# Performance work log

Hardware: AMD Instinct MI355X
Metric: run time of the kernel (lower is better)

Reference implementation:

```python
import jax, jax.numpy as jnp
import numpy as np
import math

H, W = 512, 1024
PS = 2
H_p, W_p = H // PS, W // PS
N = 9
C_IN, C_OUT = 128, 64
GROUPS = 32
B = 2
EPS_GN = 1e-5


def _make_grid():
    # Replicates LatDeform2xDown buffers: centers + sec(lat)-scaled 3x3 offsets.
    pr = np.arange(H_p, dtype=np.float32) * PS + (PS - 1) / 2
    pc = np.arange(W_p, dtype=np.float32) * PS + (PS - 1) / 2
    cy = pr / (H - 1) * 2 - 1
    cx = pc / (W - 1) * 2 - 1
    centers = np.stack([np.broadcast_to(cx[None, :], (H_p, W_p)),
                        np.broadcast_to(cy[:, None], (H_p, W_p))], axis=-1)  # (H_p,W_p,2)
    delta = math.pi / (H - 1)  # drop_south_pole = False
    lat = math.pi / 2 - pr * delta
    sec_max = W / 4.0
    sec = np.clip(1.0 / np.cos(lat), -sec_max, sec_max).astype(np.float32)
    ky, kx = np.meshgrid(np.array([-1.0, 0.0, 1.0], np.float32),
                         np.array([-1.0, 0.0, 1.0], np.float32), indexing='ij')
    kxf, kyf = kx.flatten(), ky.flatten()
    dx = (kxf[None, :] * sec[:, None]) / (W - 1) * 2          # (H_p, 9)
    dy = np.broadcast_to(kyf[None, :], (H_p, N)) / (H - 1) * 2  # (H_p, 9)
    offsets = np.stack([dx, dy], axis=-1)                      # (H_p, 9, 2)
    locs = centers[:, :, None, :] + offsets[:, None, :, :]     # (H_p, W_p, 9, 2)
    return jnp.asarray(locs.reshape(-1, 2).astype(np.float32))


def group_norm(x, gamma, beta, groups, eps=EPS_GN):
    b, c, h, w = x.shape
    xg = x.reshape(b, groups, c // groups, h, w)
    mu = xg.mean(axis=(2, 3, 4), keepdims=True)
    var = ((xg - mu) ** 2).mean(axis=(2, 3, 4), keepdims=True)
    xn = ((xg - mu) * jax.lax.rsqrt(var + eps)).reshape(b, c, h, w)
    return xn * gamma[None, :, None, None] + beta[None, :, None, None]


def setup_inputs() -> dict:
    key = jax.random.key(0)
    ks = jax.random.split(key, 3)
    x = jax.random.normal(ks[0], (B, C_IN, H_p, W_p), dtype=jnp.float32)
    w_conv = jax.random.normal(ks[1], (N * C_OUT, C_IN), dtype=jnp.float32) * 0.02
    w_post = jax.random.normal(ks[2], (C_OUT, C_OUT), dtype=jnp.float32) * 0.05
    return {
        'x': x,
        'grid': _make_grid(),
        'gamma1': jnp.ones((C_IN,), jnp.float32),
        'beta1': jnp.zeros((C_IN,), jnp.float32),
        'w_conv': w_conv,
        'splat_bias': jnp.zeros((C_OUT,), jnp.float32),
        'w_post': w_post,
        'b_post': jnp.zeros((C_OUT,), jnp.float32),
        'gamma2': jnp.ones((C_OUT,), jnp.float32),
        'beta2': jnp.zeros((C_OUT,), jnp.float32),
    }


def reference(x, grid, gamma1, beta1, w_conv, splat_bias, w_post, b_post, gamma2, beta2):
    b = x.shape[0]
    # norm + 1x1 conv (no bias): Wx part of the Wx+b split
    h = group_norm(x, gamma1, beta1, GROUPS)
    vals = jnp.einsum('oc,bchw->bohw', w_conv, h)                 # (B, 9*C, H_p, W_p)
    vals = vals.reshape(b, C_OUT, N, H_p, W_p).transpose(0, 1, 3, 4, 2)
    vals = vals.reshape(b, C_OUT, H_p * W_p * N)                  # (B, C, M)

    # bilinear splat coordinates
    px = (grid[:, 0] + 1.0) * 0.5 * (W - 1)                       # (M,)
    py = (grid[:, 1] + 1.0) * 0.5 * (H - 1)
    x0 = jnp.floor(px).astype(jnp.int32)
    y0 = jnp.floor(py).astype(jnp.int32)
    x1, y1 = x0 + 1, y0 + 1
    fx = px - x0.astype(px.dtype)
    fy = py - y0.astype(py.dtype)
    w00 = (1 - fx) * (1 - fy)
    w01 = (1 - fx) * fy
    w10 = fx * (1 - fy)
    w11 = fx * fy
    x0w = x0 % W
    x1w = x1 % W
    half_W = W // 2

    def polar_wrap(yi, xi):
        past_n = yi < 0
        past_s = yi >= H
        yi = jnp.where(past_n, -yi, yi)
        yi = jnp.where(past_s, 2 * H - yi, yi)
        xi = jnp.where(past_n | past_s, (xi + half_W) % W, xi)
        return jnp.clip(yi, 0, H - 1), xi

    num = jnp.zeros((b, C_OUT, H * W), x.dtype)
    den = jnp.zeros((H * W,), x.dtype)  # identical across batch in the original
    for wt, yi, xi in ((w00, y0, x0w), (w01, y1, x0w), (w10, y0, x1w), (w11, y1, x1w)):
        yi, xi = polar_wrap(yi, xi)
        idx = yi * W + xi                                          # (M,)
        num = num.at[:, :, idx].add(vals * wt[None, None, :])
        den = den.at[idx].add(wt)

    out = num / jnp.clip(den, 1e-8)[None, None, :]
    out = out.reshape(b, C_OUT, H, W) + splat_bias[None, :, None, None]
    # post: 1x1 conv + GroupNorm + exact GELU
    out = jnp.einsum('oc,bchw->bohw', w_post, out) + b_post[None, :, None, None]
    out = group_norm(out, gamma2, beta2, GROUPS)
    return jax.nn.gelu(out, approximate=False)
```

## Files before the change

### kernel.cpp

```cpp
#include <hip/hip_runtime.h>
#include <cstdint>
#include <cstddef>

#define H_   512
#define W_   1024
#define HP_  256
#define WP_  512
#define NTAP 9
#define CIN  128
#define COUT 64
#define HWP  (HP_*WP_)
#define MIDX (HWP*NTAP)
#define HW_  (H_*W_)

typedef __attribute__((ext_vector_type(8))) short bhalf8_t;
typedef __attribute__((ext_vector_type(4))) float floatx4_t;

__device__ __forceinline__ unsigned short f2bf(float f) {
    unsigned u = __float_as_uint(f);
    u += 0x7fffu + ((u >> 16) & 1u);
    return (unsigned short)(u >> 16);
}
__device__ __forceinline__ unsigned cvt_pk_bf16(float lo, float hi) {
    unsigned r;
    asm("v_cvt_pk_bf16_f32 %0, %1, %2" : "=v"(r) : "v"(lo), "v"(hi));
    return r;
}

__global__ __launch_bounds__(256) void k0_prep(
    const float* __restrict__ w_conv, const float* __restrict__ w_post,
    const float* __restrict__ sbias,  const float* __restrict__ b_post,
    float* __restrict__ wfold, float* __restrict__ sb2,
    float* __restrict__ gnzero ) {
    int idx = blockIdx.x * 256 + threadIdx.x;
    if (idx < 73728) {
        int r = idx >> 7, ci = idx & 127;
        int n = r >> 6, o = r & 63;
        float acc = 0.f;
        #pragma unroll 8
        for (int op = 0; op < 64; ++op)
            acc = fmaf(w_post[o*64 + op], w_conv[(op*9 + n)*128 + ci], acc);
        wfold[idx] = acc;
    } else if (idx < 73728 + 64) {
        int o = idx - 73728;
        float acc = b_post[o];
        for (int op = 0; op < 64; ++op)
            acc = fmaf(w_post[o*64 + op], sbias[op], acc);
        sb2[o] = acc;
    } else if (idx < 73728 + 64 + 256) {
        gnzero[idx - (73728 + 64)] = 0.f;
    }
}

__global__ __launch_bounds__(256) void k1_stats(const float* __restrict__ x,
                                                float* __restrict__ gnsum1) {
    __shared__ float red[512];
    int bid = blockIdx.x;
    int b = bid >> 8, rem = bid & 255;
    int g = rem >> 3, slice = rem & 7;
    const float4* xp = (const float4*)x + (size_t)(b*CIN + g*4) * (HWP/4) + (size_t)slice*16384;
    float s = 0.f, s2 = 0.f;
    for (int i = threadIdx.x; i < 16384; i += 256) {
        float4 v = xp[i];
        s  += v.x + v.y + v.z + v.w;
        s2 += v.x*v.x + v.y*v.y + v.z*v.z + v.w*v.w;
    }
    red[threadIdx.x] = s; red[256 + threadIdx.x] = s2;
    __syncthreads();
    for (int off = 128; off > 0; off >>= 1) {
        if (threadIdx.x < off) {
            red[threadIdx.x] += red[threadIdx.x + off];
            red[256 + threadIdx.x] += red[256 + threadIdx.x + off];
        }
        __syncthreads();
    }
    if (threadIdx.x == 0) {
        atomicAdd(&gnsum1[(b*32 + g)*2],     red[0]);
        atomicAdd(&gnsum1[(b*32 + g)*2 + 1], red[256]);
    }
}

__global__ void k1b_coef(const float* __restrict__ gnsum1,
                         const float* __restrict__ gamma1, const float* __restrict__ beta1,
                         float* __restrict__ acoef, float* __restrict__ bcoef) {
    int t = threadIdx.x;
    int b = t >> 7, c = t & 127, g = c >> 2;
    float s1 = gnsum1[(b*32+g)*2], s2 = gnsum1[(b*32+g)*2+1];
    const float inv = 1.f / 524288.f;
    float mean = s1 * inv;
    float var  = s2 * inv - mean*mean;
    float rstd = rsqrtf(var + 1e-5f);
    float a = gamma1[c] * rstd;
    acoef[t] = a;
    bcoef[t] = beta1[c] - mean * a;
}

__global__ __launch_bounds__(256) void k1c_scale(
    const float* __restrict__ wfold, const float* __restrict__ acoef,
    const float* __restrict__ bcoef,
    unsigned short* __restrict__ w2b, float* __restrict__ vb) {
    int b = blockIdx.y;
    int idx = blockIdx.x * 256 + threadIdx.x;
    if (idx < 73728) {
        int c = idx & 127;
        w2b[b*73728 + idx] = f2bf(wfold[idx] * acoef[b*128 + c]);
    } else if (idx < 73728 + 576) {
        int r = idx - 73728;
        float acc = 0.f;
        #pragma unroll 8
        for (int c = 0; c < 128; ++c)
            acc = fmaf(wfold[r*128 + c], bcoef[b*128 + c], acc);
        vb[b*576 + r] = acc;
    }
}

__global__ __launch_bounds__(256) void k2_conv(
    const float* __restrict__ x, const unsigned short* __restrict__ w2b,
    const float* __restrict__ vb,
    unsigned short* __restrict__ vals) {
    __shared__ unsigned short Bs[128*136];
    __shared__ unsigned short Cs[128*72];
    int b   = blockIdx.y;
    int tile = blockIdx.x;
    int pr  = tile >> 2, pcb = (tile & 3) << 7;
    int tid = threadIdx.x;

    for (int task = tid; task < 2048; task += 256) {
        int p = task & 127, c0 = (task >> 7) << 3;
        const float* xp = &x[(size_t)(b*CIN + c0)*HWP + (size_t)pr*WP_ + pcb + p];
        float v0 = xp[0];
        float v1 = xp[HWP];
        float v2 = xp[2*HWP];
        float v3 = xp[3*HWP];
        float v4 = xp[4*HWP];
        float v5 = xp[5*HWP];
        float v6 = xp[6*HWP];
        float v7 = xp[7*HWP];
        uint4 t;
        t.x = cvt_pk_bf16(v0, v1);
        t.y = cvt_pk_bf16(v2, v3);
        t.z = cvt_pk_bf16(v4, v5);
        t.w = cvt_pk_bf16(v6, v7);
        *(uint4*)&Bs[p*136 + c0] = t;
    }
    __syncthreads();

    int wave = tid >> 6, lane = tid & 63;
    int l15 = lane & 15, lq = lane >> 4;

    bhalf8_t bfr[2][4];
    #pragma unroll
    for (int ptl = 0; ptl < 2; ++ptl) {
        int p = (wave*2 + ptl)*16 + l15;
        #pragma unroll
        for (int ks = 0; ks < 4; ++ks)
            bfr[ptl][ks] = *(const bhalf8_t*)&Bs[p*136 + ks*32 + lq*8];
    }

    const unsigned short* wb = w2b + (size_t)b*73728;
    const float* vbb = vb + b*576;

    for (int n = 0; n < 9; ++n) {
        floatx4_t acc[2][4];
        #pragma unroll
        for (int rt = 0; rt < 4; ++rt) {
            float4 vbv = *(const float4*)&vbb[n*64 + rt*16 + lq*4];
            floatx4_t a0; a0[0] = vbv.x; a0[1] = vbv.y; a0[2] = vbv.z; a0[3] = vbv.w;
            acc[0][rt] = a0; acc[1][rt] = a0;
        }
        #pragma unroll
        for (int ks = 0; ks < 4; ++ks) {
            bhalf8_t af[4];
            #pragma unroll
            for (int rt = 0; rt < 4; ++rt)
                af[rt] = *(const bhalf8_t*)&wb[(n*64 + rt*16 + l15)*128 + ks*32 + lq*8];
            #pragma unroll
            for (int ptl = 0; ptl < 2; ++ptl)
                #pragma unroll
                for (int rt = 0; rt < 4; ++rt)
                    acc[ptl][rt] = __builtin_amdgcn_mfma_f32_16x16x32_bf16(
                        af[rt], bfr[ptl][ks], acc[ptl][rt], 0, 0, 0);
        }
        __syncthreads();
        #pragma unroll
        for (int ptl = 0; ptl < 2; ++ptl) {
            int p = (wave*2 + ptl)*16 + l15;
            #pragma unroll
            for (int rt = 0; rt < 4; ++rt) {
                uint2 d;
                d.x = cvt_pk_bf16(acc[ptl][rt][0], acc[ptl][rt][1]);
                d.y = cvt_pk_bf16(acc[ptl][rt][2], acc[ptl][rt][3]);
                *(uint2*)&Cs[p*72 + rt*16 + lq*4] = d;
            }
        }
        __syncthreads();
        size_t outbase = (size_t)b*HWP + (size_t)pr*WP_ + pcb;
        for (int i = tid; i < 4096; i += 256) {
            int p = i >> 5, o2 = i & 31;
            ((unsigned*)vals)[((outbase + p)*576 + n*64)/2 + o2] = ((const unsigned*)Cs)[p*36 + o2];
        }
    }
}

__global__ __launch_bounds__(256) void k3_gather(
    const float* __restrict__ gridp, const unsigned short* __restrict__ vals,
    const float* __restrict__ sb2g,
    float* __restrict__ out, float* __restrict__ gnsum2) {

    __shared__ float sb2_s[64];
    __shared__ float red[256];

    int tid = threadIdx.x;
    int bx = blockIdx.x;
    int y  = blockIdx.y;
    int b  = blockIdx.z;
    int x  = (bx << 8) + tid;

    if (tid < 64) sb2_s[tid] = sb2g[tid];
    __syncthreads();

    float num[64];
    #pragma unroll
    for (int c = 0; c < 64; ++c) num[c] = 0.f;
    float den = 0.f;

    const float2* g2 = (const float2*)gridp;
    int prc = y >> 1;
    for (int dpr = -1; dpr <= 1; ++dpr) {
        int pr = prc + dpr;
        if (pr < 0 || pr > HP_-1) continue;
        for (int kyi = 0; kyi < 3; ++kyi) {
            float gy = g2[pr*WP_*9 + kyi*3 + 1].y;
            float py = ((gy + 1.0f) * 0.5f) * 511.0f;
            float y0f = floorf(py);
            float fy = py - y0f;
            int y0i = (int)y0f;
            #pragma unroll
            for (int side = 0; side < 2; ++side) {
                int yi = y0i + side;
                bool pn = yi < 0, ps = yi >= H_;
                int yy = pn ? -yi : (ps ? (2*H_ - yi) : yi);
                yy = min(max(yy, 0), H_-1);
                if (yy != y) continue;
                int sh = (pn || ps) ? (W_/2) : 0;
                float wy = side ? fy : (1.0f - fy);
                for (int kxi = 0; kxi < 3; ++kxi) {
                    int n = kyi*3 + kxi;
                    float gx0 = g2[pr*WP_*9 + n].x;
                    float px0 = ((gx0 + 1.0f) * 0.5f) * 1023.0f;
                    int Tt = x - sh - 1;
                    #pragma unroll
                    for (int j = -1; j <= 1; ++j) {
                        float A = ((float)(Tt + j*W_) - px0) * 0.5f;
                        int clo = (int)ceilf(A - 1e-3f);
                        int chi = (int)floorf(A + 1.001f);
                        for (int pc = clo; pc <= chi; ++pc) {
                            if (pc < 0 || pc >= WP_) continue;
                            int m = (pr*WP_ + pc)*9 + n;
                            float2 g = g2[m];
                            float px = ((g.x + 1.0f) * 0.5f) * 1023.0f;
                            float x0f = floorf(px);
                            float fx = px - x0f;
                            int x0i = (int)x0f;
                            int xl = (x0i + 2*W_ + sh) & (W_-1);
                            float w;
                            if (xl == x)                      w = (1.0f - fx) * wy;
                            else if (((xl + 1) & (W_-1)) == x) w = fx * wy;
                            else continue;
                            den += w;
                            const uint4* vp = (const uint4*)(vals + (((size_t)b*MIDX + m) << 6));
                            #pragma unroll
                            for (int q = 0; q < 8; ++q) {
                                uint4 u = vp[q];
                                unsigned uu[4] = {u.x, u.y, u.z, u.w};
                                #pragma unroll
                                for (int e = 0; e < 4; ++e) {
                                    float lo = __uint_as_float(uu[e] << 16);
                                    float hi = __uint_as_float(uu[e] & 0xffff0000u);
                                    num[q*8 + e*2]     = fmaf(w, lo, num[q*8 + e*2]);
                                    num[q*8 + e*2 + 1] = fmaf(w, hi, num[q*8 + e*2 + 1]);
                                }
                            }
                        }
                    }
                }
            }
        }
    }

    float invd = 1.0f / fmaxf(den, 1e-8f);
    size_t obase = ((size_t)b << 25) + ((size_t)y << 10) + (size_t)x;
    #pragma unroll
    for (int c = 0; c < 64; ++c) {
        float v = fmaf(num[c], invd, sb2_s[c]);
        out[obase + ((size_t)c << 19)] = v;
        num[c] = v;
    }

    float st[64];
    #pragma unroll
    for (int g = 0; g < 32; ++g) {
        float a = num[2*g], b2 = num[2*g + 1];
        st[g]      = a + b2;
        st[32 + g] = fmaf(a, a, b2*b2);
    }
    int lane = tid & 63;
    float r32[32];
    { bool hi = (lane & 32) != 0;
      #pragma unroll
      for (int j = 0; j < 32; ++j) {
          float keep = hi ? st[32+j] : st[j];
          float send = hi ? st[j]    : st[32+j];
          r32[j] = keep + __shfl_xor(send, 32, 64);
      } }
    float r16[16];
    { bool hi = (lane & 16) != 0;
      #pragma unroll
      for (int j = 0; j < 16; ++j) {
          float keep = hi ? r32[16+j] : r32[j];
          float send = hi ? r32[j]    : r32[16+j];
          r16[j] = keep + __shfl_xor(send, 16, 64);
      } }
    float r8[8];
    { bool hi = (lane & 8) != 0;
      #pragma unroll
      for (int j = 0; j < 8; ++j) {
          float keep = hi ? r16[8+j] : r16[j];
          float send = hi ? r16[j]   : r16[8+j];
          r8[j] = keep + __shfl_xor(send, 8, 64);
      } }
    float r4[4];
    { bool hi = (lane & 4) != 0;
      #pragma unroll
      for (int j = 0; j < 4; ++j) {
          float keep = hi ? r8[4+j] : r8[j];
          float send = hi ? r8[j]   : r8[4+j];
          r4[j] = keep + __shfl_xor(send, 4, 64);
      } }
    float r2[2];
    { bool hi = (lane & 2) != 0;
      #pragma unroll
      for (int j = 0; j < 2; ++j) {
          float keep = hi ? r4[2+j] : r4[j];
          float send = hi ? r4[j]   : r4[2+j];
          r2[j] = keep + __shfl_xor(send, 2, 64);
      } }
    float r1;
    { bool hi = (lane & 1) != 0;
      float keep = hi ? r2[1] : r2[0];
      float send = hi ? r2[0] : r2[1];
      r1 = keep + __shfl_xor(send, 1, 64);
    }
    red[tid] = r1;
    __syncthreads();
    if (tid < 64) {
        float tot = red[tid] + red[tid + 64] + red[tid + 128] + red[tid + 192];
        int slot = (tid < 32) ? (tid << 1) : (((tid - 32) << 1) + 1);
        atomicAdd(&gnsum2[(b << 6) + slot], tot);
    }
}

__global__ __launch_bounds__(256) void k5_final(
    float* __restrict__ out, const float* __restrict__ gnsum2,
    const float* __restrict__ gamma2, const float* __restrict__ beta2) {
    size_t idx = (size_t)blockIdx.x * 256 + threadIdx.x;
    size_t e8 = idx << 3;
    int b = (int)(e8 >> 25);
    int o = (int)((e8 >> 19) & 63);
    int g = o >> 1;
    float s1 = gnsum2[b*64 + g*2], s2 = gnsum2[b*64 + g*2 + 1];
    const float invn = 1.0f / 1048576.0f;
    float mean = s1 * invn;
    float var  = s2 * invn - mean*mean;
    float rstd = rsqrtf(var + 1e-5f);
    float sc = gamma2[o] * rstd;
    float sf = beta2[o] - mean * sc;
    float4* p0 = (float4*)(out + e8);
    float4 v0 = p0[0], v1 = p0[1];
    float r[8] = {v0.x, v0.y, v0.z, v0.w, v1.x, v1.y, v1.z, v1.w};
    #pragma unroll
    for (int j = 0; j < 8; ++j) {
        float t = fmaf(r[j], sc, sf);
        r[j] = 0.5f * t * (1.0f + erff(t * 0.70710678118654752f));
    }
    p0[0] = make_float4(r[0], r[1], r[2], r[3]);
    p0[1] = make_float4(r[4], r[5], r[6], r[7]);
}

extern "C" void kernel_launch(void* const* d_in, const int* in_sizes, int n_in,
                              void* d_out, int out_size, void* d_ws, size_t ws_size,
                              hipStream_t stream) {
    const float* x      = (const float*)d_in[0];
    const float* gridp  = (const float*)d_in[1];
    const float* gamma1 = (const float*)d_in[2];
    const float* beta1  = (const float*)d_in[3];
    const float* w_conv = (const float*)d_in[4];
    const float* sbias  = (const float*)d_in[5];
    const float* w_post = (const float*)d_in[6];
    const float* b_post = (const float*)d_in[7];
    const float* gamma2 = (const float*)d_in[8];
    const float* beta2  = (const float*)d_in[9];
    float* out = (float*)d_out;

    char* ws = (char*)d_ws;
    float* wfold  = (float*)(ws);
    unsigned short* w2b = (unsigned short*)(ws + 294912);
    float* vb     = (float*)(ws + 589824);
    float* gnsum1 = (float*)(ws + 594432);
    float* gnsum2 = (float*)(ws + 594944);
    float* acoef  = (float*)(ws + 595456);
    float* bcoef  = (float*)(ws + 596480);
    float* sb2    = (float*)(ws + 597504);
    unsigned short* vals = (unsigned short*)(ws + 597760);

    hipLaunchKernelGGL(k0_prep,  dim3(290),          dim3(256), 0, stream,
                       w_conv, w_post, sbias, b_post, wfold, sb2, gnsum1);
    hipLaunchKernelGGL(k1_stats, dim3(512),          dim3(256), 0, stream, x, gnsum1);
    hipLaunchKernelGGL(k1b_coef, dim3(1),            dim3(256), 0, stream,
                       gnsum1, gamma1, beta1, acoef, bcoef);
    hipLaunchKernelGGL(k1c_scale, dim3(291, 2),      dim3(256), 0, stream,
                       wfold, acoef, bcoef, w2b, vb);
    hipLaunchKernelGGL(k2_conv,  dim3(1024, 2),      dim3(256), 0, stream,
                       x, w2b, vb, vals);
    hipLaunchKernelGGL(k3_gather, dim3(4, 512, 2),   dim3(256), 0, stream,
                       gridp, vals, sb2, out, gnsum2);
    hipLaunchKernelGGL(k5_final, dim3(32768),        dim3(256), 0, stream,
                       out, gnsum2, gamma2, beta2);
}
```

Before: 848.1 us.

## Split gather channels across two threads per output pixel

The gather kernel now assigns each output pixel to two adjacent threads, each accumulating 32 of the 64 channels, and the grid doubles in x to match. This halves the per-thread accumulator and reduction register arrays, which should raise occupancy and latency hiding for the scattered bf16 loads. The cost is that the tap search and weight computation are duplicated across both threads. The warp-shuffle GroupNorm reduction is re-indexed so each lane still lands on the correct group-statistic slot.

Result: slower. 871.8 us (+2.8%).

```diff
diff --git a/kernel.cpp b/kernel.cpp
--- a/kernel.cpp
+++ b/kernel.cpp
@@ -214,14 +214,15 @@
     int bx = blockIdx.x;
     int y  = blockIdx.y;
     int b  = blockIdx.z;
-    int x  = (bx << 8) + tid;
+    int h  = tid & 1;
+    int x  = (bx << 7) + (tid >> 1);
 
     if (tid < 64) sb2_s[tid] = sb2g[tid];
     __syncthreads();
 
-    float num[64];
+    float num[32];
     #pragma unroll
-    for (int c = 0; c < 64; ++c) num[c] = 0.f;
+    for (int c = 0; c < 32; ++c) num[c] = 0.f;
     float den = 0.f;
 
     const float2* g2 = (const float2*)gridp;
@@ -268,9 +269,9 @@
                             else if (((xl + 1) & (W_-1)) == x) w = fx * wy;
                             else continue;
                             den += w;
-                            const uint4* vp = (const uint4*)(vals + (((size_t)b*MIDX + m) << 6));
+                            const uint4* vp = (const uint4*)(vals + (((size_t)b*MIDX + m) << 6) + (h << 5));
                             #pragma unroll
-                            for (int q = 0; q < 8; ++q) {
+                            for (int q = 0; q < 4; ++q) {
                                 uint4 u = vp[q];
                                 unsigned uu[4] = {u.x, u.y, u.z, u.w};
                                 #pragma unroll
@@ -289,73 +290,68 @@
     }
 
     float invd = 1.0f / fmaxf(den, 1e-8f);
+    int ch0 = h << 5;
     size_t obase = ((size_t)b << 25) + ((size_t)y << 10) + (size_t)x;
     #pragma unroll
-    for (int c = 0; c < 64; ++c) {
-        float v = fmaf(num[c], invd, sb2_s[c]);
-        out[obase + ((size_t)c << 19)] = v;
+    for (int c = 0; c < 32; ++c) {
+        float v = fmaf(num[c], invd, sb2_s[ch0 + c]);
+        out[obase + ((size_t)(ch0 + c) << 19)] = v;
         num[c] = v;
     }
 
-    float st[64];
+    float st[32];
     #pragma unroll
-    for (int g = 0; g < 32; ++g) {
-        float a = num[2*g], b2 = num[2*g + 1];
-        st[g]      = a + b2;
-        st[32 + g] = fmaf(a, a, b2*b2);
+    for (int gg = 0; gg < 16; ++gg) {
+        float a = num[2*gg], b2 = num[2*gg + 1];
+        st[gg]      = a + b2;
+        st[16 + gg] = fmaf(a, a, b2*b2);
     }
     int lane = tid & 63;
-    float r32[32];
+    float r16[16];
     { bool hi = (lane & 32) != 0;
       #pragma unroll
-      for (int j = 0; j < 32; ++j) {
-          float keep = hi ? st[32+j] : st[j];
-          float send = hi ? st[j]    : st[32+j];
-          r32[j] = keep + __shfl_xor(send, 32, 64);
-      } }
-    float r16[16];
-    { bool hi = (lane & 16) != 0;
-      #pragma unroll
       for (int j = 0; j < 16; ++j) {
-          float keep = hi ? r32[16+j] : r32[j];
-          float send = hi ? r32[j]    : r32[16+j];
-          r16[j] = keep + __shfl_xor(send, 16, 64);
+          float keep = hi ? st[16+j] : st[j];
+          float send = hi ? st[j]    : st[16+j];
+          r16[j] = keep + __shfl_xor(send, 32, 64);
       } }
     float r8[8];
-    { bool hi = (lane & 8) != 0;
+    { bool hi = (lane & 16) != 0;
       #pragma unroll
       for (int j = 0; j < 8; ++j) {
           float keep = hi ? r16[8+j] : r16[j];
           float send = hi ? r16[j]   : r16[8+j];
-          r8[j] = keep + __shfl_xor(send, 8, 64);
+          r8[j] = keep + __shfl_xor(send, 16, 64);
       } }
     float r4[4];
-    { bool hi = (lane & 4) != 0;
+    { bool hi = (lane & 8) != 0;
       #pragma unroll
       for (int j = 0; j < 4; ++j) {
           float keep = hi ? r8[4+j] : r8[j];
           float send = hi ? r8[j]   : r8[4+j];
-          r4[j] = keep + __shfl_xor(send, 4, 64);
+          r4[j] = keep + __shfl_xor(send, 8, 64);
       } }
     float r2[2];
-    { bool hi = (lane & 2) != 0;
+    { bool hi = (lane & 4) != 0;
       #pragma unroll
       for (int j = 0; j < 2; ++j) {
           float keep = hi ? r4[2+j] : r4[j];
           float send = hi ? r4[j]   : r4[2+j];
-          r2[j] = keep + __shfl_xor(send, 2, 64);
+          r2[j] = keep + __shfl_xor(send, 4, 64);
       } }
     float r1;
-    { bool hi = (lane & 1) != 0;
+    { bool hi = (lane & 2) != 0;
       float keep = hi ? r2[1] : r2[0];
       float send = hi ? r2[0] : r2[1];
-      r1 = keep + __shfl_xor(send, 1, 64);
+      r1 = keep + __shfl_xor(send, 2, 64);
     }
     red[tid] = r1;
     __syncthreads();
     if (tid < 64) {
         float tot = red[tid] + red[tid + 64] + red[tid + 128] + red[tid + 192];
-        int slot = (tid < 32) ? (tid << 1) : (((tid - 32) << 1) + 1);
+        int p = tid & 1, k = tid >> 1;
+        int g = (p << 4) + (k & 15);
+        int slot = g*2 + (k >> 4);
         atomicAdd(&gnsum2[(b << 6) + slot], tot);
     }
 }
@@ -422,7 +418,7 @@
                        wfold, acoef, bcoef, w2b, vb);
     hipLaunchKernelGGL(k2_conv,  dim3(1024, 2),      dim3(256), 0, stream,
                        x, w2b, vb, vals);
-    hipLaunchKernelGGL(k3_gather, dim3(4, 512, 2),   dim3(256), 0, stream,
+    hipLaunchKernelGGL(k3_gather, dim3(8, 512, 2),   dim3(256), 0, stream,
                        gridp, vals, sb2, out, gnsum2);
     hipLaunchKernelGGL(k5_final, dim3(32768),        dim3(256), 0, stream,
                        out, gnsum2, gamma2, beta2);
```

## Defer gather contributions to LDS list and double-buffer value loads

Applied to the files above, without the earlier changes.

The gather kernel now records each contributing (index, weight) pair in a per-thread shared-memory list of up to 24 entries, rather than loading and accumulating the 128-byte value vector inside the discovery loop. A second loop then walks the list with two register buffers, issuing the next vector's loads before consuming the current one so that global memory latency overlaps with the FMAs. This adds 48KB of LDS per block and 64 extra registers for the buffers, which may cut occupancy. Entries beyond 24 fall back to the old inline path.

Result: no change. 849.7 us (+0.2%).

```diff
diff --git a/kernel.cpp b/kernel.cpp
--- a/kernel.cpp
+++ b/kernel.cpp
@@ -12,6 +12,7 @@
 #define HWP  (HP_*WP_)
 #define MIDX (HWP*NTAP)
 #define HW_  (H_*W_)
+#define LK   24
 
 typedef __attribute__((ext_vector_type(8))) short bhalf8_t;
 typedef __attribute__((ext_vector_type(4))) float floatx4_t;
@@ -202,11 +203,34 @@
     }
 }
 
+__device__ __forceinline__ float issue8(const unsigned short* __restrict__ vbase,
+                                        const uint2* __restrict__ lp, uint4* buf) {
+    uint2 e = *lp;
+    const uint4* vp = (const uint4*)(vbase + ((size_t)e.x << 6));
+    #pragma unroll
+    for (int q = 0; q < 8; ++q) buf[q] = vp[q];
+    return __uint_as_float(e.y);
+}
+__device__ __forceinline__ void consume8(const uint4* buf, float w, float* num) {
+    #pragma unroll
+    for (int q = 0; q < 8; ++q) {
+        unsigned uu[4] = {buf[q].x, buf[q].y, buf[q].z, buf[q].w};
+        #pragma unroll
+        for (int e = 0; e < 4; ++e) {
+            float lo = __uint_as_float(uu[e] << 16);
+            float hi = __uint_as_float(uu[e] & 0xffff0000u);
+            num[q*8 + e*2]     = fmaf(w, lo, num[q*8 + e*2]);
+            num[q*8 + e*2 + 1] = fmaf(w, hi, num[q*8 + e*2 + 1]);
+        }
+    }
+}
+
 __global__ __launch_bounds__(256) void k3_gather(
     const float* __restrict__ gridp, const unsigned short* __restrict__ vals,
     const float* __restrict__ sb2g,
     float* __restrict__ out, float* __restrict__ gnsum2) {
 
+    __shared__ uint2 lst[LK*256];
     __shared__ float sb2_s[64];
     __shared__ float red[256];
 
@@ -223,8 +247,11 @@
     #pragma unroll
     for (int c = 0; c < 64; ++c) num[c] = 0.f;
     float den = 0.f;
+    int cnt = 0;
 
     const float2* g2 = (const float2*)gridp;
+    const unsigned short* vbase = vals + (((size_t)b*MIDX) << 6);
+
     int prc = y >> 1;
     for (int dpr = -1; dpr <= 1; ++dpr) {
         int pr = prc + dpr;
@@ -268,23 +295,40 @@
                             else if (((xl + 1) & (W_-1)) == x) w = fx * wy;
                             else continue;
                             den += w;
-                            const uint4* vp = (const uint4*)(vals + (((size_t)b*MIDX + m) << 6));
-                            #pragma unroll
-                            for (int q = 0; q < 8; ++q) {
-                                uint4 u = vp[q];
-                                unsigned uu[4] = {u.x, u.y, u.z, u.w};
+                            if (cnt < LK) {
+                                lst[cnt*256 + tid] = make_uint2((unsigned)m, __float_as_uint(w));
+                                ++cnt;
+                            } else {
+                                const uint4* vp = (const uint4*)(vbase + ((size_t)m << 6));
                                 #pragma unroll
-                                for (int e = 0; e < 4; ++e) {
-                                    float lo = __uint_as_float(uu[e] << 16);
-                                    float hi = __uint_as_float(uu[e] & 0xffff0000u);
-                                    num[q*8 + e*2]     = fmaf(w, lo, num[q*8 + e*2]);
-                                    num[q*8 + e*2 + 1] = fmaf(w, hi, num[q*8 + e*2 + 1]);
+                                for (int q = 0; q < 8; ++q) {
+                                    uint4 u = vp[q];
+                                    unsigned uu[4] = {u.x, u.y, u.z, u.w};
+                                    #pragma unroll
+                                    for (int e = 0; e < 4; ++e) {
+                                        float lo = __uint_as_float(uu[e] << 16);
+                                        float hi = __uint_as_float(uu[e] & 0xffff0000u);
+                                        num[q*8 + e*2]     = fmaf(w, lo, num[q*8 + e*2]);
+                                        num[q*8 + e*2 + 1] = fmaf(w, hi, num[q*8 + e*2 + 1]);
+                                    }
                                 }
                             }
                         }
                     }
                 }
             }
+        }
+    }
+
+    {
+        uint4 bufA[8], bufB[8];
+        float wA = 0.f, wB = 0.f;
+        if (cnt > 0) wA = issue8(vbase, &lst[tid], bufA);
+        for (int i = 0; i < cnt; i += 2) {
+            if (i + 1 < cnt) wB = issue8(vbase, &lst[(i+1)*256 + tid], bufB);
+            consume8(bufA, wA, num);
+            if (i + 2 < cnt) wA = issue8(vbase, &lst[(i+2)*256 + tid], bufA);
+            if (i + 1 < cnt) consume8(bufB, wB, num);
         }
     }
 
```
